# Kernel tuning notes

Measured on AMD Instinct MI355X. Metric: run time of the kernel, lower is better.

The kernel has to match this reference:

```python
import jax, jax.numpy as jnp
import numpy as np

DIM = 96; HEADS = 3; HEAD_DIM = 32; INNER = HEADS * HEAD_DIM; MLP = 384
WS = 4; WV = WS ** 3; SHIFT = WS // 2  # displacement = window//2
SPATIAL = 64


def _rel_indices():
    c = np.stack(np.meshgrid(np.arange(WS), np.arange(WS), np.arange(WS), indexing='ij'), -1).reshape(-1, 3)
    return c[:, None] - c[None, :] + (WS - 1)  # [WV, WV, 3] in [0, 2*WS-2]

REL = _rel_indices()


def _make_mask():
    # standard Swin shifted-window mask: label contiguity regions, partition, -inf cross-region
    X = Y = Z = SPATIAL
    lab = np.zeros((X, Y, Z), np.int32); cnt = 0
    sl = (slice(0, -WS), slice(-WS, -SHIFT), slice(-SHIFT, None))
    for sx in sl:
        for sy in sl:
            for sz in sl:
                lab[sx, sy, sz] = cnt; cnt += 1
    n = X // WS
    lab = lab.reshape(n, WS, n, WS, n, WS).transpose(0, 2, 4, 1, 3, 5).reshape(-1, WV)
    m = np.where(lab[:, :, None] != lab[:, None, :], -1e9, 0.0).astype(np.float32)
    return jnp.asarray(m)  # [nW, WV, WV]

MASK = _make_mask()


def _ln(x, g, b):
    m = x.mean(-1, keepdims=True)
    v = ((x - m) ** 2).mean(-1, keepdims=True)
    return (x - m) * jax.lax.rsqrt(v + 1e-5) * g + b


def _window_attn(x, W_qkv, W_out, b_out, pos_tab):
    B, X, Y, Z, _ = x.shape
    x = jnp.roll(x, (-SHIFT, -SHIFT, -SHIFT), axis=(1, 2, 3))  # cyclic shift
    qkv = x @ W_qkv  # [B,X,Y,Z,3*INNER]
    nx, ny, nz = X // WS, Y // WS, Z // WS
    qkv = qkv.reshape(B, nx, WS, ny, WS, nz, WS, 3, HEADS, HEAD_DIM)
    qkv = qkv.transpose(7, 0, 8, 1, 3, 5, 2, 4, 6, 9).reshape(3, B, HEADS, nx * ny * nz, WV, HEAD_DIM)
    q, k, v = qkv[0], qkv[1], qkv[2]
    dots = jnp.einsum('bhwid,bhwjd->bhwij', q, k) * (HEAD_DIM ** -0.5)
    bias = pos_tab[REL[..., 0], REL[..., 1], REL[..., 2]]  # [WV,WV]
    dots = dots + bias + MASK[None, None]
    attn = jax.nn.softmax(dots, axis=-1)
    out = jnp.einsum('bhwij,bhwjd->bhwid', attn, v)
    out = out.reshape(B, HEADS, nx, ny, nz, WS, WS, WS, HEAD_DIM)
    out = out.transpose(0, 2, 5, 3, 6, 4, 7, 1, 8).reshape(B, X, Y, Z, INNER)
    out = out @ W_out + b_out
    return jnp.roll(out, (SHIFT, SHIFT, SHIFT), axis=(1, 2, 3))  # cyclic back-shift


def setup_inputs() -> dict:
    key = jax.random.key(0)
    ks = jax.random.split(key, 8)
    w = lambda k, shape, s=0.02: (jax.random.normal(k, shape, jnp.float32) * s)
    return {
        'x': jax.random.normal(ks[0], (1, SPATIAL, SPATIAL, SPATIAL, DIM), jnp.float32),
        'W_qkv': w(ks[1], (DIM, 3 * INNER)),
        'W_out': w(ks[2], (INNER, DIM)),
        'b_out': jnp.zeros((DIM,), jnp.float32),
        'pos_tab': w(ks[3], (2 * WS - 1, 2 * WS - 1, 2 * WS - 1), 1.0),
        'ln1_g': jnp.ones((DIM,), jnp.float32), 'ln1_b': jnp.zeros((DIM,), jnp.float32),
        'ln2_g': jnp.ones((DIM,), jnp.float32), 'ln2_b': jnp.zeros((DIM,), jnp.float32),
        'W1': w(ks[4], (DIM, MLP)), 'b1': jnp.zeros((MLP,), jnp.float32),
        'W2': w(ks[5], (MLP, DIM)), 'b2': jnp.zeros((DIM,), jnp.float32),
    }


def reference(x, W_qkv, W_out, b_out, pos_tab, ln1_g, ln1_b, ln2_g, ln2_b, W1, b1, W2, b2):
    # Residual(PreNorm(WindowAttention3D))
    x = x + _window_attn(_ln(x, ln1_g, ln1_b), W_qkv, W_out, b_out, pos_tab)
    # Residual(PreNorm(FeedForward3D)): Linear -> GELU -> Linear (dropout=0)
    h = _ln(x, ln2_g, ln2_b)
    h = jax.nn.gelu(h @ W1 + b1, approximate=False) @ W2 + b2
    return x + h
```

## Files before the change

### kernel.cpp

```cpp
#include <hip/hip_runtime.h>

typedef __attribute__((ext_vector_type(8))) short bf16x8;
typedef __attribute__((ext_vector_type(4))) short s16x4;
typedef __attribute__((ext_vector_type(4))) float f32x4;

#define NTOK 262144
#define NWIN 4096

__device__ __forceinline__ unsigned short f2bf(float f) {
    unsigned int u = __float_as_uint(f);
    return (unsigned short)((u + 0x7FFFu + ((u >> 16) & 1u)) >> 16);
}
__device__ __forceinline__ float bf2f(unsigned short u) {
    return __uint_as_float(((unsigned int)u) << 16);
}
__device__ __forceinline__ int region(int g) { return (g >= 60) + (g >= 62); }

__global__ void convert_weights(const float* __restrict__ Wqkv, const float* __restrict__ Wout,
                                const float* __restrict__ W1, const float* __restrict__ W2,
                                unsigned short* __restrict__ wq_t, unsigned short* __restrict__ wo_t,
                                unsigned short* __restrict__ w1_t, unsigned short* __restrict__ w2_t) {
    int idx = blockIdx.x * blockDim.x + threadIdx.x;
    if (idx < 27648) {
        int n = idx / 96, k = idx % 96;
        wq_t[idx] = f2bf(Wqkv[k * 288 + n]);
    } else if (idx < 27648 + 9216) {
        int i = idx - 27648; int n = i / 96, k = i % 96;
        wo_t[i] = f2bf(Wout[k * 96 + n]);
    } else if (idx < 27648 + 9216 + 36864) {
        int i = idx - 36864; int n = i / 96, k = i % 96;
        w1_t[i] = f2bf(W1[k * 384 + n]);
    } else if (idx < 110592) {
        int i = idx - 73728; int n = i / 384, k = i % 384;
        w2_t[i] = f2bf(W2[k * 96 + n]);
    }
}

__global__ __launch_bounds__(256) void ln1_shift_kernel(const float* __restrict__ x,
                                                        const float* __restrict__ g,
                                                        const float* __restrict__ b,
                                                        unsigned short* __restrict__ y) {
    int tid = blockIdx.x * blockDim.x + threadIdx.x;
    int token = tid >> 5;
    int lane = tid & 31;
    if (token >= NTOK) return;
    int pz = token & 63, py = (token >> 6) & 63, px = token >> 12;
    int sx = (px + 2) & 63, sy = (py + 2) & 63, sz = (pz + 2) & 63;
    size_t src = ((size_t)((sx * 64 + sy) * 64 + sz)) * 96;
    float v0 = x[src + lane], v1 = x[src + 32 + lane], v2 = x[src + 64 + lane];
    float s = v0 + v1 + v2;
    float sq = v0 * v0 + v1 * v1 + v2 * v2;
    #pragma unroll
    for (int m = 16; m >= 1; m >>= 1) { s += __shfl_xor(s, m, 32); sq += __shfl_xor(sq, m, 32); }
    float mean = s * (1.0f / 96.0f);
    float var = sq * (1.0f / 96.0f) - mean * mean;
    float rstd = rsqrtf(var + 1e-5f);
    int win = ((px >> 2) * 16 + (py >> 2)) * 16 + (pz >> 2);
    int loc = ((px & 3) * 4 + (py & 3)) * 4 + (pz & 3);
    size_t dst = ((size_t)(win * 64 + loc)) * 96;
    y[dst + lane]      = f2bf((v0 - mean) * rstd * g[lane]      + b[lane]);
    y[dst + 32 + lane] = f2bf((v1 - mean) * rstd * g[lane + 32] + b[lane + 32]);
    y[dst + 64 + lane] = f2bf((v2 - mean) * rstd * g[lane + 64] + b[lane + 64]);
}

__global__ __launch_bounds__(384, 4) void qkv_attn_kernel(
    const unsigned short* __restrict__ y,
    const unsigned short* __restrict__ wq_t,
    const float* __restrict__ pos_tab,
    unsigned short* __restrict__ a_out)
{
    __shared__ __align__(16) unsigned short SH[22272];
    __shared__ __align__(16) float posl[344];
    unsigned short* q_s = SH;
    unsigned short* k_s = SH + 7680;
    unsigned short* vT  = SH + 15360;
    unsigned short* P_s = SH;

    int win = blockIdx.x;
    int tid = threadIdx.x;
    int w = tid >> 6, lane = tid & 63, lr = lane & 15, kh = lane >> 4;
    int ix = win >> 8, iy = (win >> 4) & 15, iz = win & 15;

    if (tid < 343) posl[tid] = pos_tab[tid];

    {
        f32x4 acc3[4][3];
        #pragma unroll
        for (int m = 0; m < 4; ++m)
            #pragma unroll
            for (int n = 0; n < 3; ++n) acc3[m][n] = (f32x4){0.f, 0.f, 0.f, 0.f};
        #pragma unroll
        for (int ks = 0; ks < 3; ++ks) {
            int k0 = ks * 32;
            bf16x8 a[4], bb[3];
            #pragma unroll
            for (int m = 0; m < 4; ++m)
                a[m] = *(const bf16x8*)(y + ((size_t)win * 64 + m * 16 + lr) * 96 + k0 + kh * 8);
            #pragma unroll
            for (int n = 0; n < 3; ++n)
                bb[n] = *(const bf16x8*)(wq_t + (size_t)(w * 48 + n * 16 + lr) * 96 + k0 + kh * 8);
            #pragma unroll
            for (int m = 0; m < 4; ++m)
                #pragma unroll
                for (int n = 0; n < 3; ++n)
                    acc3[m][n] = __builtin_amdgcn_mfma_f32_16x16x32_bf16(a[m], bb[n], acc3[m][n], 0, 0, 0);
        }
        const float scale = 0.17677669529663689f;
        #pragma unroll
        for (int n = 0; n < 3; ++n) {
            int base = w * 48 + n * 16;
            int qq = base / 96, cc0 = base % 96;
            int hh = cc0 >> 5, d0 = cc0 & 31;
            if (qq == 2) {
                #pragma unroll
                for (int m = 0; m < 4; ++m) {
                    s16x4 pv;
                    #pragma unroll
                    for (int r = 0; r < 4; ++r) pv[r] = (short)f2bf(acc3[m][n][r]);
                    *(s16x4*)&vT[(hh * 32 + d0 + lr) * 72 + m * 16 + kh * 4] = pv;
                }
            } else {
                unsigned short* dst = (qq == 0) ? q_s : k_s;
                float sc = (qq == 0) ? scale : 1.0f;
                #pragma unroll
                for (int m = 0; m < 4; ++m)
                    #pragma unroll
                    for (int r = 0; r < 4; ++r) {
                        int tok = m * 16 + kh * 4 + r;
                        dst[(hh * 64 + tok) * 40 + d0 + lr] = f2bf(acc3[m][n][r] * sc);
                    }
            }
        }
    }
    __syncthreads();

    int h3 = w >> 1, rb = (w & 1) * 32;
    f32x4 sa[2][4];
    {
        bf16x8 aq[2], bk[4];
        #pragma unroll
        for (int mm = 0; mm < 2; ++mm)
            aq[mm] = *(const bf16x8*)&q_s[(h3 * 64 + rb + mm * 16 + lr) * 40 + kh * 8];
        #pragma unroll
        for (int n = 0; n < 4; ++n)
            bk[n] = *(const bf16x8*)&k_s[(h3 * 64 + n * 16 + lr) * 40 + kh * 8];
        #pragma unroll
        for (int mm = 0; mm < 2; ++mm)
            #pragma unroll
            for (int n = 0; n < 4; ++n)
                sa[mm][n] = __builtin_amdgcn_mfma_f32_16x16x32_bf16(aq[mm], bk[n], (f32x4){0.f,0.f,0.f,0.f}, 0, 0, 0);

        int labj[4], jwx[4], jwy[4], jwz[4];
        #pragma unroll
        for (int n = 0; n < 4; ++n) {
            int j = n * 16 + lr;
            jwx[n] = j >> 4; jwy[n] = (j >> 2) & 3; jwz[n] = j & 3;
            labj[n] = 9 * region(ix * 4 + jwx[n]) + 3 * region(iy * 4 + jwy[n]) + region(iz * 4 + jwz[n]);
        }
        #pragma unroll
        for (int mm = 0; mm < 2; ++mm)
            #pragma unroll
            for (int r = 0; r < 4; ++r) {
                int i = rb + mm * 16 + kh * 4 + r;
                int iwx = i >> 4, iwy = (i >> 2) & 3, iwz = i & 3;
                int labi = 9 * region(ix * 4 + iwx) + 3 * region(iy * 4 + iwy) + region(iz * 4 + iwz);
                #pragma unroll
                for (int n = 0; n < 4; ++n) {
                    float bias = posl[((iwx - jwx[n] + 3) * 7 + (iwy - jwy[n] + 3)) * 7 + (iwz - jwz[n] + 3)];
                    sa[mm][n][r] += bias + (labi != labj[n] ? -1e9f : 0.0f);
                }
                float mx = fmaxf(fmaxf(sa[mm][0][r], sa[mm][1][r]), fmaxf(sa[mm][2][r], sa[mm][3][r]));
                #pragma unroll
                for (int s = 1; s < 16; s <<= 1) mx = fmaxf(mx, __shfl_xor(mx, s, 16));
                float e0 = __expf(sa[mm][0][r] - mx), e1 = __expf(sa[mm][1][r] - mx);
                float e2 = __expf(sa[mm][2][r] - mx), e3 = __expf(sa[mm][3][r] - mx);
                float sum = e0 + e1 + e2 + e3;
                #pragma unroll
                for (int s = 1; s < 16; s <<= 1) sum += __shfl_xor(sum, s, 16);
                float rs = 1.0f / sum;
                sa[mm][0][r] = e0 * rs; sa[mm][1][r] = e1 * rs;
                sa[mm][2][r] = e2 * rs; sa[mm][3][r] = e3 * rs;
            }
    }
    __syncthreads();

    #pragma unroll
    for (int mm = 0; mm < 2; ++mm)
        #pragma unroll
        for (int n = 0; n < 4; ++n)
            #pragma unroll
            for (int r = 0; r < 4; ++r)
                P_s[(h3 * 64 + rb + mm * 16 + kh * 4 + r) * 72 + n * 16 + lr] = f2bf(sa[mm][n][r]);
    __syncthreads();

    {
        f32x4 oa[2][2];
        #pragma unroll
        for (int mm = 0; mm < 2; ++mm)
            #pragma unroll
            for (int n = 0; n < 2; ++n) oa[mm][n] = (f32x4){0.f, 0.f, 0.f, 0.f};
        #pragma unroll
        for (int ks = 0; ks < 2; ++ks) {
            int k0 = ks * 32;
            bf16x8 ap[2], bv[2];
            #pragma unroll
            for (int mm = 0; mm < 2; ++mm)
                ap[mm] = *(const bf16x8*)&P_s[(h3 * 64 + rb + mm * 16 + lr) * 72 + k0 + kh * 8];
            #pragma unroll
            for (int n = 0; n < 2; ++n)
                bv[n] = *(const bf16x8*)&vT[(h3 * 32 + n * 16 + lr) * 72 + k0 + kh * 8];
            #pragma unroll
            for (int mm = 0; mm < 2; ++mm)
                #pragma unroll
                for (int n = 0; n < 2; ++n)
                    oa[mm][n] = __builtin_amdgcn_mfma_f32_16x16x32_bf16(ap[mm], bv[n], oa[mm][n], 0, 0, 0);
        }
        #pragma unroll
        for (int mm = 0; mm < 2; ++mm)
            #pragma unroll
            for (int n = 0; n < 2; ++n)
                #pragma unroll
                for (int r = 0; r < 4; ++r) {
                    int tok = rb + mm * 16 + kh * 4 + r;
                    a_out[((size_t)win * 64 + tok) * 96 + h3 * 32 + n * 16 + lr] = f2bf(oa[mm][n][r]);
                }
    }
}

__global__ __launch_bounds__(256, 4) void proj_mlp5_kernel(
    const unsigned short* __restrict__ a_out,
    const unsigned short* __restrict__ wo_t, const float* __restrict__ b_out,
    const float* __restrict__ x,
    const float* __restrict__ g2, const float* __restrict__ bt2,
    const unsigned short* __restrict__ w1_t, const float* __restrict__ b1,
    const unsigned short* __restrict__ w2_t, const float* __restrict__ b2,
    float* __restrict__ out)
{
    __shared__ __align__(16) unsigned short SH[13312];
    unsigned short* xl = SH;
    unsigned short* gl = SH + 6656;
    float* tile = (float*)SH;

    int win = blockIdx.x;
    int tid = threadIdx.x;
    int w = tid >> 6, lane = tid & 63, lr = lane & 15, kh = lane >> 4;
    int ix = win >> 8, iy = (win >> 4) & 15, iz = win & 15;
    int tb = w * 16;

    int px = (ix * 4 + w + 2) & 63;
    int py = (iy * 4 + kh + 2) & 63;
    int rowbase = (px * 64 + py) * 64;
    int o[4];
    #pragma unroll
    for (int r = 0; r < 4; ++r) o[r] = (rowbase + ((iz * 4 + r + 2) & 63)) * 96;

    float x1v[6][4];
    {
        f32x4 pa[6];
        #pragma unroll
        for (int n = 0; n < 6; ++n) pa[n] = (f32x4){0.f, 0.f, 0.f, 0.f};
        #pragma unroll
        for (int ks = 0; ks < 3; ++ks) {
            int k0 = ks * 32;
            bf16x8 a = *(const bf16x8*)(a_out + ((size_t)win * 64 + tb + lr) * 96 + k0 + kh * 8);
            #pragma unroll
            for (int n = 0; n < 6; ++n) {
                bf16x8 bb = *(const bf16x8*)(wo_t + (size_t)(n * 16 + lr) * 96 + k0 + kh * 8);
                pa[n] = __builtin_amdgcn_mfma_f32_16x16x32_bf16(a, bb, pa[n], 0, 0, 0);
            }
        }
        #pragma unroll
        for (int n = 0; n < 6; ++n) {
            int c = n * 16 + lr;
            float bo = b_out[c];
            #pragma unroll
            for (int r = 0; r < 4; ++r)
                x1v[n][r] = x[o[r] + c] + pa[n][r] + bo;
        }
        float g2c[6], bc2[6];
        #pragma unroll
        for (int n = 0; n < 6; ++n) { g2c[n] = g2[n * 16 + lr]; bc2[n] = bt2[n * 16 + lr]; }
        #pragma unroll
        for (int r = 0; r < 4; ++r) {
            float s = 0.f, sq = 0.f;
            #pragma unroll
            for (int n = 0; n < 6; ++n) { s += x1v[n][r]; sq += x1v[n][r] * x1v[n][r]; }
            #pragma unroll
            for (int m = 8; m >= 1; m >>= 1) { s += __shfl_xor(s, m, 16); sq += __shfl_xor(sq, m, 16); }
            float mean = s * (1.0f / 96.0f);
            float var = sq * (1.0f / 96.0f) - mean * mean;
            float rstd = rsqrtf(var + 1e-5f);
            int t = tb + kh * 4 + r;
            #pragma unroll
            for (int n = 0; n < 6; ++n)
                xl[t * 104 + n * 16 + lr] = f2bf((x1v[n][r] - mean) * rstd * g2c[n] + bc2[n]);
        }
    }
    __syncthreads();

    int wm = w & 1, wn = w >> 1;
    f32x4 acc2[2][3];
    #pragma unroll
    for (int mf = 0; mf < 2; ++mf)
        #pragma unroll
        for (int nf = 0; nf < 3; ++nf) acc2[mf][nf] = (f32x4){0.f, 0.f, 0.f, 0.f};

    for (int ch = 0; ch < 4; ++ch) {
        f32x4 a1[2][3];
        #pragma unroll
        for (int mf = 0; mf < 2; ++mf)
            #pragma unroll
            for (int nf = 0; nf < 3; ++nf) a1[mf][nf] = (f32x4){0.f, 0.f, 0.f, 0.f};
        #pragma unroll
        for (int ks = 0; ks < 3; ++ks) {
            int k0 = ks * 32;
            bf16x8 af[2], bfr[3];
            #pragma unroll
            for (int mf = 0; mf < 2; ++mf)
                af[mf] = *(const bf16x8*)&xl[(wm * 32 + mf * 16 + lr) * 104 + k0 + kh * 8];
            #pragma unroll
            for (int nf = 0; nf < 3; ++nf)
                bfr[nf] = *(const bf16x8*)(w1_t + (size_t)(ch * 96 + wn * 48 + nf * 16 + lr) * 96 + k0 + kh * 8);
            #pragma unroll
            for (int mf = 0; mf < 2; ++mf)
                #pragma unroll
                for (int nf = 0; nf < 3; ++nf)
                    a1[mf][nf] = __builtin_amdgcn_mfma_f32_16x16x32_bf16(af[mf], bfr[nf], a1[mf][nf], 0, 0, 0);
        }
        #pragma unroll
        for (int nf = 0; nf < 3; ++nf) {
            int lcol = wn * 48 + nf * 16 + lr;
            float bias = b1[ch * 96 + lcol];
            #pragma unroll
            for (int mf = 0; mf < 2; ++mf)
                #pragma unroll
                for (int r = 0; r < 4; ++r) {
                    float u = a1[mf][nf][r] + bias;
                    float t = 1.5957691216057308f * (u + 0.044715f * u * u * u);
                    float ge = u * __builtin_amdgcn_rcpf(1.0f + __expf(-t));
                    gl[(wm * 32 + mf * 16 + kh * 4 + r) * 104 + lcol] = f2bf(ge);
                }
        }
        __syncthreads();
        #pragma unroll
        for (int kc = 0; kc < 3; ++kc) {
            int k0 = kc * 32;
            bf16x8 ag[2];
            #pragma unroll
            for (int mf = 0; mf < 2; ++mf)
                ag[mf] = *(const bf16x8*)&gl[(wm * 32 + mf * 16 + lr) * 104 + k0 + kh * 8];
            #pragma unroll
            for (int nf = 0; nf < 3; ++nf) {
                bf16x8 bb = *(const bf16x8*)(w2_t + (size_t)(wn * 48 + nf * 16 + lr) * 384 + ch * 96 + k0 + kh * 8);
                #pragma unroll
                for (int mf = 0; mf < 2; ++mf)
                    acc2[mf][nf] = __builtin_amdgcn_mfma_f32_16x16x32_bf16(ag[mf], bb, acc2[mf][nf], 0, 0, 0);
            }
        }
        __syncthreads();
    }

    #pragma unroll
    for (int r = 0; r < 4; ++r) {
        int t = tb + kh * 4 + r;
        #pragma unroll
        for (int n = 0; n < 6; ++n)
            tile[t * 100 + n * 16 + lr] = x1v[n][r];
    }
    __syncthreads();
    #pragma unroll
    for (int nf = 0; nf < 3; ++nf) {
        int col = wn * 48 + nf * 16 + lr;
        float bc = b2[col];
        #pragma unroll
        for (int mf = 0; mf < 2; ++mf)
            #pragma unroll
            for (int r = 0; r < 4; ++r) {
                int row = wm * 32 + mf * 16 + kh * 4 + r;
                tile[row * 100 + col] += acc2[mf][nf][r] + bc;
            }
    }
    __syncthreads();
    #pragma unroll
    for (int j = 0; j < 6; ++j) {
        int f4 = j * 256 + tid;
        int token = f4 / 24, c4 = f4 % 24;
        int wx = token >> 4, wy = (token >> 2) & 3, wz = token & 3;
        int qx = (ix * 4 + wx + 2) & 63, qy = (iy * 4 + wy + 2) & 63, qz = (iz * 4 + wz + 2) & 63;
        size_t g = ((size_t)((qx * 64 + qy) * 64 + qz)) * 96 + c4 * 4;
        f32x4 v = *(const f32x4*)&tile[token * 100 + c4 * 4];
        *(f32x4*)&out[g] = v;
    }
}

extern "C" void kernel_launch(void* const* d_in, const int* in_sizes, int n_in,
                              void* d_out, int out_size, void* d_ws, size_t ws_size,
                              hipStream_t stream) {
    const float* x       = (const float*)d_in[0];
    const float* Wqkv    = (const float*)d_in[1];
    const float* Wout    = (const float*)d_in[2];
    const float* b_out   = (const float*)d_in[3];
    const float* pos_tab = (const float*)d_in[4];
    const float* ln1_g   = (const float*)d_in[5];
    const float* ln1_b   = (const float*)d_in[6];
    const float* ln2_g   = (const float*)d_in[7];
    const float* ln2_b   = (const float*)d_in[8];
    const float* W1      = (const float*)d_in[9];
    const float* b1      = (const float*)d_in[10];
    const float* W2      = (const float*)d_in[11];
    const float* b2      = (const float*)d_in[12];
    float* out = (float*)d_out;

    char* ws = (char*)d_ws;
    unsigned short* y     = (unsigned short*)(ws);
    unsigned short* a_out = (unsigned short*)(ws + 50331648);
    unsigned short* wq_t  = (unsigned short*)(ws + 100663296);
    unsigned short* wo_t  = wq_t + 27648;
    unsigned short* w1_t  = wo_t + 9216;
    unsigned short* w2_t  = w1_t + 36864;

    convert_weights<<<432, 256, 0, stream>>>(Wqkv, Wout, W1, W2, wq_t, wo_t, w1_t, w2_t);
    ln1_shift_kernel<<<32768, 256, 0, stream>>>(x, ln1_g, ln1_b, y);
    qkv_attn_kernel<<<NWIN, 384, 0, stream>>>(y, wq_t, pos_tab, a_out);
    proj_mlp5_kernel<<<NWIN, 256, 0, stream>>>(a_out, wo_t, b_out, x,
                                               ln2_g, ln2_b, w1_t, b1, w2_t, b2, out);
}
```

Before: 264.5 us.

## Fuse LayerNorm and cyclic shift into the QKV attention kernel

```diff
diff --git a/kernel.cpp b/kernel.cpp
--- a/kernel.cpp
+++ b/kernel.cpp
@@ -4,7 +4,6 @@
 typedef __attribute__((ext_vector_type(4))) short s16x4;
 typedef __attribute__((ext_vector_type(4))) float f32x4;
 
-#define NTOK 262144
 #define NWIN 4096
 
 __device__ __forceinline__ unsigned short f2bf(float f) {
@@ -36,35 +35,9 @@
     }
 }
 
-__global__ __launch_bounds__(256) void ln1_shift_kernel(const float* __restrict__ x,
-                                                        const float* __restrict__ g,
-                                                        const float* __restrict__ b,
-                                                        unsigned short* __restrict__ y) {
-    int tid = blockIdx.x * blockDim.x + threadIdx.x;
-    int token = tid >> 5;
-    int lane = tid & 31;
-    if (token >= NTOK) return;
-    int pz = token & 63, py = (token >> 6) & 63, px = token >> 12;
-    int sx = (px + 2) & 63, sy = (py + 2) & 63, sz = (pz + 2) & 63;
-    size_t src = ((size_t)((sx * 64 + sy) * 64 + sz)) * 96;
-    float v0 = x[src + lane], v1 = x[src + 32 + lane], v2 = x[src + 64 + lane];
-    float s = v0 + v1 + v2;
-    float sq = v0 * v0 + v1 * v1 + v2 * v2;
-    #pragma unroll
-    for (int m = 16; m >= 1; m >>= 1) { s += __shfl_xor(s, m, 32); sq += __shfl_xor(sq, m, 32); }
-    float mean = s * (1.0f / 96.0f);
-    float var = sq * (1.0f / 96.0f) - mean * mean;
-    float rstd = rsqrtf(var + 1e-5f);
-    int win = ((px >> 2) * 16 + (py >> 2)) * 16 + (pz >> 2);
-    int loc = ((px & 3) * 4 + (py & 3)) * 4 + (pz & 3);
-    size_t dst = ((size_t)(win * 64 + loc)) * 96;
-    y[dst + lane]      = f2bf((v0 - mean) * rstd * g[lane]      + b[lane]);
-    y[dst + 32 + lane] = f2bf((v1 - mean) * rstd * g[lane + 32] + b[lane + 32]);
-    y[dst + 64 + lane] = f2bf((v2 - mean) * rstd * g[lane + 64] + b[lane + 64]);
-}
-
-__global__ __launch_bounds__(384, 4) void qkv_attn_kernel(
-    const unsigned short* __restrict__ y,
+__global__ __launch_bounds__(384, 4) void ln_qkv_attn_kernel(
+    const float* __restrict__ x,
+    const float* __restrict__ ln1_g, const float* __restrict__ ln1_b,
     const unsigned short* __restrict__ wq_t,
     const float* __restrict__ pos_tab,
     unsigned short* __restrict__ a_out)
@@ -74,6 +47,7 @@
     unsigned short* q_s = SH;
     unsigned short* k_s = SH + 7680;
     unsigned short* vT  = SH + 15360;
+    unsigned short* y_s = SH + 15360;
     unsigned short* P_s = SH;
 
     int win = blockIdx.x;
@@ -84,7 +58,35 @@
     if (tid < 343) posl[tid] = pos_tab[tid];
 
     {
-        f32x4 acc3[4][3];
+        int grp = tid >> 4, gi = tid & 15;
+        float gv[6], bv[6];
+        #pragma unroll
+        for (int j = 0; j < 6; ++j) { gv[j] = ln1_g[gi + 16 * j]; bv[j] = ln1_b[gi + 16 * j]; }
+        #pragma unroll
+        for (int p = 0; p < 3; ++p) {
+            int t = grp + p * 24;
+            if (t < 64) {
+                int wx = t >> 4, wy = (t >> 2) & 3, wz = t & 3;
+                int sx = (ix * 4 + wx + 2) & 63, sy = (iy * 4 + wy + 2) & 63, sz = (iz * 4 + wz + 2) & 63;
+                const float* src = x + ((size_t)((sx * 64 + sy) * 64 + sz)) * 96;
+                float v[6]; float s = 0.f, sq = 0.f;
+                #pragma unroll
+                for (int j = 0; j < 6; ++j) { v[j] = src[gi + 16 * j]; s += v[j]; sq += v[j] * v[j]; }
+                #pragma unroll
+                for (int m = 8; m >= 1; m >>= 1) { s += __shfl_xor(s, m, 16); sq += __shfl_xor(sq, m, 16); }
+                float mean = s * (1.0f / 96.0f);
+                float var = sq * (1.0f / 96.0f) - mean * mean;
+                float rstd = rsqrtf(var + 1e-5f);
+                #pragma unroll
+                for (int j = 0; j < 6; ++j)
+                    y_s[t * 104 + gi + 16 * j] = f2bf((v[j] - mean) * rstd * gv[j] + bv[j]);
+            }
+        }
+    }
+    __syncthreads();
+
+    f32x4 acc3[4][3];
+    {
         #pragma unroll
         for (int m = 0; m < 4; ++m)
             #pragma unroll
@@ -95,7 +97,7 @@
             bf16x8 a[4], bb[3];
             #pragma unroll
             for (int m = 0; m < 4; ++m)
-                a[m] = *(const bf16x8*)(y + ((size_t)win * 64 + m * 16 + lr) * 96 + k0 + kh * 8);
+                a[m] = *(const bf16x8*)&y_s[(m * 16 + lr) * 104 + k0 + kh * 8];
             #pragma unroll
             for (int n = 0; n < 3; ++n)
                 bb[n] = *(const bf16x8*)(wq_t + (size_t)(w * 48 + n * 16 + lr) * 96 + k0 + kh * 8);
@@ -105,6 +107,10 @@
                 for (int n = 0; n < 3; ++n)
                     acc3[m][n] = __builtin_amdgcn_mfma_f32_16x16x32_bf16(a[m], bb[n], acc3[m][n], 0, 0, 0);
         }
+    }
+    __syncthreads();
+
+    {
         const float scale = 0.17677669529663689f;
         #pragma unroll
         for (int n = 0; n < 3; ++n) {
@@ -412,16 +418,14 @@
     float* out = (float*)d_out;
 
     char* ws = (char*)d_ws;
-    unsigned short* y     = (unsigned short*)(ws);
-    unsigned short* a_out = (unsigned short*)(ws + 50331648);
-    unsigned short* wq_t  = (unsigned short*)(ws + 100663296);
+    unsigned short* a_out = (unsigned short*)(ws);
+    unsigned short* wq_t  = (unsigned short*)(ws + 50331648);
     unsigned short* wo_t  = wq_t + 27648;
     unsigned short* w1_t  = wo_t + 9216;
     unsigned short* w2_t  = w1_t + 36864;
 
     convert_weights<<<432, 256, 0, stream>>>(Wqkv, Wout, W1, W2, wq_t, wo_t, w1_t, w2_t);
-    ln1_shift_kernel<<<32768, 256, 0, stream>>>(x, ln1_g, ln1_b, y);
-    qkv_attn_kernel<<<NWIN, 384, 0, stream>>>(y, wq_t, pos_tab, a_out);
+    ln_qkv_attn_kernel<<<NWIN, 384, 0, stream>>>(x, ln1_g, ln1_b, wq_t, pos_tab, a_out);
     proj_mlp5_kernel<<<NWIN, 256, 0, stream>>>(a_out, wo_t, b_out, x,
                                                ln2_g, ln2_b, w1_t, b1, w2_t, b2, out);
 }
```

New measurement: 233.4 us. 11.8% less time.
